# Optimization experiments

Measured on AMD Instinct MI355X. Metric: run time of the kernel, lower is better.

## Reference

```python
import jax, jax.numpy as jnp
import numpy as np

EPS = 1e-3  # keras LayerNormalization default epsilon

def _layernorm(x, g, b):
    mu = jnp.mean(x, axis=-1, keepdims=True)
    var = jnp.mean(jnp.square(x - mu), axis=-1, keepdims=True)
    return (x - mu) * jax.lax.rsqrt(var + EPS) * g + b

def setup_inputs() -> dict:
    key = jax.random.key(0)
    ks = jax.random.split(key, 12)
    B, T, C = 2, 2048, 768
    s = 0.02
    return {
        "x": jax.random.normal(ks[0], (B, T, C), jnp.float32),
        "ln1_g": jnp.ones((C,), jnp.float32), "ln1_b": jnp.zeros((C,), jnp.float32),
        "Wq": jax.random.normal(ks[1], (C, C), jnp.float32) * s, "bq": jnp.zeros((C,), jnp.float32),
        "Wk": jax.random.normal(ks[2], (C, C), jnp.float32) * s, "bk": jnp.zeros((C,), jnp.float32),
        "Wv": jax.random.normal(ks[3], (C, C), jnp.float32) * s, "bv": jnp.zeros((C,), jnp.float32),
        "ln2_g": jnp.ones((C,), jnp.float32), "ln2_b": jnp.zeros((C,), jnp.float32),
        "W1": jax.random.normal(ks[4], (C, 4 * C), jnp.float32) * s, "b1": jnp.zeros((4 * C,), jnp.float32),
        "W2": jax.random.normal(ks[5], (4 * C, C), jnp.float32) * s, "b2": jnp.zeros((C,), jnp.float32),
    }

def reference(x, ln1_g, ln1_b, Wq, bq, Wk, bk, Wv, bv, ln2_g, ln2_b, W1, b1, W2, b2):
    H = 12
    B, T, C = x.shape
    dh = C // H
    # pre-LN (note: original overwrites x with LN output before residual)
    x = _layernorm(x, ln1_g, ln1_b)
    q = (x @ Wq + bq).reshape(B, T, H, dh).transpose(0, 2, 1, 3)
    k = (x @ Wk + bk).reshape(B, T, H, dh).transpose(0, 2, 1, 3)
    v = (x @ Wv + bv).reshape(B, T, H, dh).transpose(0, 2, 1, 3)
    # original computes K @ Q^T (transpose_b on query)
    scores = jnp.einsum('bhid,bhjd->bhij', k, q) / jnp.sqrt(jnp.float32(dh))
    mask = jnp.tril(jnp.ones((T, T), bool))
    scores = jnp.where(mask, scores, -jnp.inf)
    p = jax.nn.softmax(scores, axis=-1)
    y = jnp.einsum('bhij,bhjd->bhid', p, v)  # [B,H,T,dh]
    y = y.transpose(0, 2, 1, 3).reshape(B, T, C)
    x = x + y
    h = _layernorm(x, ln2_g, ln2_b)
    h = jax.nn.gelu(h @ W1 + b1, approximate=False)
    h = h @ W2 + b2
    return x + h
```

## Files before the change

### kernel.cpp

```cpp
#include <hip/hip_runtime.h>
#include <hip/hip_bf16.h>
#include <cmath>


#define BB 2
#define TT 2048
#define CC 768
#define HH 12
#define DH 64
#define NROWS (BB*TT)

typedef __attribute__((ext_vector_type(8))) short bf16x8;
typedef __attribute__((ext_vector_type(4))) float f32x4;
typedef __attribute__((ext_vector_type(4))) unsigned short u16x4;

__device__ __forceinline__ unsigned short f2bf(float f){
  union { __hip_bfloat16 h; unsigned short u; } c;
  c.h = __float2bfloat16(f);
  return c.u;
}
__device__ __forceinline__ float bf2f(unsigned short u){
  union { unsigned int i; float f; } x; x.i = ((unsigned int)u) << 16; return x.f;
}
__device__ __forceinline__ int swz(int r, int c){
  int b = (r << 7) + (c << 1);
  b ^= (r & 7) << 4;
  return b >> 1;
}
__device__ __forceinline__ float wred_sum(float v){
  #pragma unroll
  for(int m = 1; m < 64; m <<= 1) v += __shfl_xor(v, m, 64);
  return v;
}
__device__ __forceinline__ float gelu_exact(float x){
  return 0.5f * x * (1.0f + erff(x * 0.70710678118654752f));
}
__device__ __forceinline__ void gload_lds16(const void* g, void* l){
  __builtin_amdgcn_global_load_lds((const __attribute__((address_space(1))) void*)g,
                                   (__attribute__((address_space(3))) void*)l, 16, 0, 0);
}
template<int N> __device__ __forceinline__ void waitcnt_vm(){
  if constexpr (N == 0)      asm volatile("s_waitcnt vmcnt(0)" ::: "memory");
  else if constexpr (N == 4) asm volatile("s_waitcnt vmcnt(4)" ::: "memory");
  else if constexpr (N == 8) asm volatile("s_waitcnt vmcnt(8)" ::: "memory");
  else static_assert(N == 0 || N == 4 || N == 8, "unsupported vmcnt");
}

__device__ __forceinline__ void tc_body(const float* __restrict__ in,
                                        unsigned short* __restrict__ out,
                                        int K, int N, int bx, int by,
                                        float (*tile)[33]){
  int n0 = bx * 32, k0 = by * 32;
  int t = threadIdx.x; int c = t & 31; int r0 = t >> 5;
  #pragma unroll
  for(int p = 0; p < 4; p++){
    int r = r0 + p * 8;
    tile[r][c] = in[(size_t)(k0 + r) * N + n0 + c];
  }
  __syncthreads();
  #pragma unroll
  for(int p = 0; p < 4; p++){
    int r = r0 + p * 8;
    out[(size_t)(n0 + r) * K + k0 + c] = f2bf(tile[c][r]);
  }
}

__device__ __forceinline__ void ln_body(const float* __restrict__ in,
                                        const float* __restrict__ gm,
                                        const float* __restrict__ bt,
                                        unsigned short* __restrict__ out_b,
                                        int r){
  int t = threadIdx.x;
  const float* row = in + (size_t)r * CC;
  float v0 = row[t], v1 = row[t + 256], v2 = row[t + 512];
  float s = wred_sum(v0 + v1 + v2);
  __shared__ float red[4];
  if((t & 63) == 0) red[t >> 6] = s;
  __syncthreads();
  float mu = (red[0] + red[1] + red[2] + red[3]) * (1.0f / CC);
  float d0 = v0 - mu, d1 = v1 - mu, d2 = v2 - mu;
  float q = wred_sum(d0 * d0 + d1 * d1 + d2 * d2);
  __shared__ float red2[4];
  if((t & 63) == 0) red2[t >> 6] = q;
  __syncthreads();
  float var = (red2[0] + red2[1] + red2[2] + red2[3]) * (1.0f / CC);
  float rinv = rsqrtf(var + 1e-3f);
  float o0 = d0 * rinv * gm[t]       + bt[t];
  float o1 = d1 * rinv * gm[t + 256] + bt[t + 256];
  float o2 = d2 * rinv * gm[t + 512] + bt[t + 512];
  size_t base = (size_t)r * CC;
  out_b[base + t] = f2bf(o0); out_b[base + t + 256] = f2bf(o1); out_b[base + t + 512] = f2bf(o2);
}

__global__ __launch_bounds__(256) void prep_ln_kernel(const float* __restrict__ Wq,
                                                      const float* __restrict__ Wk,
                                                      const float* __restrict__ Wv,
                                                      const float* __restrict__ W1,
                                                      const float* __restrict__ W2,
                                                      const float* __restrict__ bq,
                                                      const float* __restrict__ bk,
                                                      const float* __restrict__ bv,
                                                      const float* __restrict__ x,
                                                      const float* __restrict__ ln1g,
                                                      const float* __restrict__ ln1b,
                                                      unsigned short* __restrict__ wqkv,
                                                      unsigned short* __restrict__ w1t,
                                                      unsigned short* __restrict__ w2t,
                                                      float* __restrict__ bqkv,
                                                      unsigned short* __restrict__ xlnb){
  __shared__ float tile[32][33];
  int o = blockIdx.x;
  if(o < 1728){
    int z = o / 576, r = o % 576;
    const float* in = (z == 0) ? Wq : (z == 1) ? Wk : Wv;
    tc_body(in, wqkv + (size_t)z * CC * CC, CC, CC, r % 24, r / 24, tile);
  } else if(o < 4032){
    int r = o - 1728;
    tc_body(W1, w1t, CC, 4 * CC, r % 96, r / 96, tile);
  } else if(o < 6336){
    int r = o - 4032;
    tc_body(W2, w2t, 4 * CC, CC, r % 24, r / 24, tile);
  } else if(o < 6345){
    int i = (o - 6336) * 256 + threadIdx.x;
    if(i < 3 * CC) bqkv[i] = (i < CC) ? bq[i] : (i < 2 * CC) ? bk[i - CC] : bv[i - 2 * CC];
  } else {
    ln_body(x, ln1g, ln1b, xlnb, o - 6345);
  }
}

__global__ __launch_bounds__(256) void ln_kernel(const float* __restrict__ in,
                                                 const float* __restrict__ gm,
                                                 const float* __restrict__ bt,
                                                 unsigned short* __restrict__ out_b){
  ln_body(in, gm, bt, out_b, blockIdx.x);
}

template<int MODE, int TILE>
__global__ __launch_bounds__(256) void gemm_bt(const unsigned short* __restrict__ A,
                                               const unsigned short* __restrict__ Bt,
                                               const float* __restrict__ bias,
                                               const float* __restrict__ resid,
                                               void* __restrict__ outp,
                                               int M, int N, int K){
  constexpr int F = TILE / 32;
  constexpr int R = TILE / 32;
  constexpr int NLD = 2 * R;
  __shared__ unsigned short As[2][TILE * 64];
  __shared__ unsigned short Bs[2][TILE * 64];
  int m0 = blockIdx.y * TILE, n0 = blockIdx.x * TILE;
  int t = threadIdx.x; int w = t >> 6; int l = t & 63;
  int g = l >> 4; int lc = l & 15;
  int wm = w >> 1, wn = w & 1;
  f32x4 zero4 = {0.f, 0.f, 0.f, 0.f};
  f32x4 acc[F][F];
  #pragma unroll
  for(int mi = 0; mi < F; mi++)
    #pragma unroll
    for(int ni = 0; ni < F; ni++) acc[mi][ni] = zero4;

  auto stage = [&](int ks, int cb){
    #pragma unroll
    for(int p = 0; p < R; p++){
      int e = (w * R + p) * 512 + l * 8;
      int r = e >> 6, clin = e & 63;
      int csrc = clin ^ ((r & 7) << 3);
      gload_lds16(A  + (size_t)(m0 + r) * K + ks + csrc, &As[cb][(w * R + p) * 512]);
      gload_lds16(Bt + (size_t)(n0 + r) * K + ks + csrc, &Bs[cb][(w * R + p) * 512]);
    }
  };

  int nt = K >> 6;
  stage(0, 0);
  if(nt > 1) stage(64, 1);
  for(int ti = 0; ti < nt; ti++){
    if(ti + 1 < nt) waitcnt_vm<NLD>(); else waitcnt_vm<0>();
    __builtin_amdgcn_s_barrier();
    int cur = ti & 1;
    #pragma unroll
    for(int kk = 0; kk < 2; kk++){
      bf16x8 af[F], bfv[F];
      #pragma unroll
      for(int mi = 0; mi < F; mi++) af[mi]  = *(const bf16x8*)&As[cur][swz(wm * (TILE / 2) + mi * 16 + lc, kk * 32 + g * 8)];
      #pragma unroll
      for(int ni = 0; ni < F; ni++) bfv[ni] = *(const bf16x8*)&Bs[cur][swz(wn * (TILE / 2) + ni * 16 + lc, kk * 32 + g * 8)];
      #pragma unroll
      for(int mi = 0; mi < F; mi++)
        #pragma unroll
        for(int ni = 0; ni < F; ni++)
          acc[mi][ni] = __builtin_amdgcn_mfma_f32_16x16x32_bf16(af[mi], bfv[ni], acc[mi][ni], 0, 0, 0);
    }
    __builtin_amdgcn_s_barrier();
    if(ti + 2 < nt) stage((ti + 2) << 6, cur);
  }
  #pragma unroll
  for(int mi = 0; mi < F; mi++)
    #pragma unroll
    for(int ni = 0; ni < F; ni++){
      int col = n0 + wn * (TILE / 2) + ni * 16 + lc;
      float bvv = bias[col];
      #pragma unroll
      for(int rr = 0; rr < 4; rr++){
        int row = m0 + wm * (TILE / 2) + mi * 16 + g * 4 + rr;
        float v = acc[mi][ni][rr] + bvv;
        size_t idx = (size_t)row * N + col;
        if(MODE == 1) v = gelu_exact(v);
        if(MODE == 2) ((float*)outp)[idx] = v + resid[idx];
        else          ((unsigned short*)outp)[idx] = f2bf(v);
      }
    }
}

__global__ __launch_bounds__(256) void transpose_v(const unsigned short* __restrict__ qkv,
                                                   unsigned short* __restrict__ vt){
  __shared__ unsigned short tile[64][65];
  int t0 = blockIdx.x * 64; int bh = blockIdx.y;
  int b = bh / HH, h = bh % HH;
  int t = threadIdx.x;
  #pragma unroll
  for(int p = 0; p < 2; p++){
    int idx = p * 256 + t; int r = idx >> 3; int c = (idx & 7) * 8;
    bf16x8 v = *(const bf16x8*)(qkv + (size_t)(b * TT + t0 + r) * (3 * CC) + 2 * CC + h * DH + c);
    #pragma unroll
    for(int e = 0; e < 8; e++) tile[r][c + e] = (unsigned short)v[e];
  }
  __syncthreads();
  #pragma unroll
  for(int p = 0; p < 2; p++){
    int idx = p * 256 + t; int d = idx >> 3; int c = (idx & 7) * 8;
    bf16x8 v;
    #pragma unroll
    for(int e = 0; e < 8; e++) v[e] = (short)tile[c + e][d];
    *(bf16x8*)(vt + (size_t)(bh * DH + d) * TT + t0 + c) = v;
  }
}

__global__ __launch_bounds__(256) void attn_kernel(const unsigned short* __restrict__ qkv,
                                                   const unsigned short* __restrict__ vt,
                                                   const unsigned short* __restrict__ xlnb,
                                                   float* __restrict__ x1){
  __shared__ unsigned short Aq[2][64 * 64];
  __shared__ unsigned short Vs[2][64 * 64];
  __shared__ unsigned short Ps[4][16 * 64];
  int o = blockIdx.x;
  int xcd = o & 7, qq = o >> 3;
  int head = xcd * 3 + (qq % 3);
  int bx = 31 - qq / 3;
  int b = head / HH, h = head % HH;
  int t = threadIdx.x; int w = t >> 6; int l = t & 63;
  int g = l >> 4, lc = l & 15;
  int i0w = bx * 64 + w * 16;
  int irow = i0w + lc;
  unsigned short* pw = &Ps[w][0];
  const float SC = 0.125f * 1.44269504f;

  int rl = l >> 3;
  int csrc = ((l & 7) * 8) ^ (rl * 8);

  bf16x8 bk[2];
  #pragma unroll
  for(int kk = 0; kk < 2; kk++)
    bk[kk] = *(const bf16x8*)(qkv + (size_t)(b * TT + irow) * (3 * CC) + CC + h * DH + kk * 32 + g * 8);

  float m_ = 0.0f, lsum = 0.f;
  f32x4 zero4 = {0.f, 0.f, 0.f, 0.f};
  f32x4 o4[4];
  #pragma unroll
  for(int ds = 0; ds < 4; ds++) o4[ds] = zero4;

  int NJT_w = (i0w + 16 + 63) >> 6;
  int NJTmax = bx + 1;

  auto stage = [&](int j0, int cb){
    #pragma unroll
    for(int p = 0; p < 2; p++){
      int sgi = w * 2 + p;
      int row = sgi * 8 + rl;
      gload_lds16(qkv + (size_t)(b * TT + j0 + row) * (3 * CC) + h * DH + csrc, &Aq[cb][sgi * 512]);
      gload_lds16(vt  + (size_t)(head * DH + row) * TT + j0 + csrc,             &Vs[cb][sgi * 512]);
    }
  };

  stage(0, 0);
  if(NJTmax > 1) stage(64, 1);

  for(int jt = 0; jt < NJTmax; jt++){
    int j0 = jt * 64;
    int buf = jt & 1;
    if(jt + 1 < NJTmax) waitcnt_vm<4>(); else waitcnt_vm<0>();
    __builtin_amdgcn_s_barrier();
    if(jt < NJT_w){
      f32x4 s[4];
      __builtin_amdgcn_s_setprio(1);
      #pragma unroll
      for(int js = 0; js < 4; js++){
        s[js] = zero4;
        #pragma unroll
        for(int kk = 0; kk < 2; kk++){
          bf16x8 aq = *(const bf16x8*)&Aq[buf][swz(js * 16 + lc, kk * 32 + g * 8)];
          s[js] = __builtin_amdgcn_mfma_f32_16x16x32_bf16(aq, bk[kk], s[js], 0, 0, 0);
        }
      }
      __builtin_amdgcn_s_setprio(0);
      if(j0 + 63 > i0w){
        #pragma unroll
        for(int js = 0; js < 4; js++)
          #pragma unroll
          for(int rr = 0; rr < 4; rr++){
            int j = j0 + js * 16 + g * 4 + rr;
            if(j > irow) s[js][rr] = -1e30f;
          }
      }
      float nmSC = -m_ * SC;
      f32x4 p[4];
      float rsum = 0.f;
      #pragma unroll
      for(int js = 0; js < 4; js++)
        #pragma unroll
        for(int rr = 0; rr < 4; rr++){
          float pv = exp2f(fmaf(s[js][rr], SC, nmSC));
          p[js][rr] = pv;
          rsum += pv;
        }
      rsum += __shfl_xor(rsum, 16, 64);
      rsum += __shfl_xor(rsum, 32, 64);
      if(__builtin_expect(__any(!(rsum < 1e30f)), 0)){
        float mx = -1e30f;
        #pragma unroll
        for(int js = 0; js < 4; js++)
          #pragma unroll
          for(int rr = 0; rr < 4; rr++) mx = fmaxf(mx, s[js][rr]);
        mx = fmaxf(mx, __shfl_xor(mx, 16, 64));
        mx = fmaxf(mx, __shfl_xor(mx, 32, 64));
        float mn = fmaxf(m_, mx);
        float al = exp2f((m_ - mn) * SC);
        m_ = mn;
        lsum *= al;
        #pragma unroll
        for(int rr = 0; rr < 4; rr++){
          float alb = __shfl(al, g * 4 + rr, 64);
          #pragma unroll
          for(int ds = 0; ds < 4; ds++) o4[ds][rr] *= alb;
        }
        nmSC = -m_ * SC;
        rsum = 0.f;
        #pragma unroll
        for(int js = 0; js < 4; js++)
          #pragma unroll
          for(int rr = 0; rr < 4; rr++){
            float pv = exp2f(fmaf(s[js][rr], SC, nmSC));
            p[js][rr] = pv;
            rsum += pv;
          }
        rsum += __shfl_xor(rsum, 16, 64);
        rsum += __shfl_xor(rsum, 32, 64);
      }
      lsum += rsum;
      #pragma unroll
      for(int js = 0; js < 4; js++){
        u16x4 pk;
        #pragma unroll
        for(int rr = 0; rr < 4; rr++) pk[rr] = f2bf(p[js][rr]);
        *(u16x4*)&pw[swz(lc, js * 16 + g * 4)] = pk;
      }
      bf16x8 pa[2];
      #pragma unroll
      for(int kk = 0; kk < 2; kk++)
        pa[kk] = *(const bf16x8*)&pw[swz(lc, kk * 32 + g * 8)];
      __builtin_amdgcn_s_setprio(1);
      #pragma unroll
      for(int ds = 0; ds < 4; ds++)
        #pragma unroll
        for(int kk = 0; kk < 2; kk++){
          bf16x8 vb = *(const bf16x8*)&Vs[buf][swz(ds * 16 + lc, kk * 32 + g * 8)];
          o4[ds] = __builtin_amdgcn_mfma_f32_16x16x32_bf16(pa[kk], vb, o4[ds], 0, 0, 0);
        }
      __builtin_amdgcn_s_setprio(0);
    }
    __builtin_amdgcn_s_barrier();
    if(jt + 2 < NJTmax) stage((jt + 2) * 64, buf);
  }
  #pragma unroll
  for(int rr = 0; rr < 4; rr++){
    float lsb = __shfl(lsum, g * 4 + rr, 64);
    float rinv = 1.0f / lsb;
    int ig = i0w + g * 4 + rr;
    #pragma unroll
    for(int ds = 0; ds < 4; ds++){
      int col = h * DH + ds * 16 + lc;
      size_t idx = (size_t)(b * TT + ig) * CC + col;
      x1[idx] = bf2f(xlnb[idx]) + o4[ds][rr] * rinv;
    }
  }
}

extern "C" void kernel_launch(void* const* d_in, const int* in_sizes, int n_in,
                              void* d_out, int out_size, void* d_ws, size_t ws_size,
                              hipStream_t stream){
  const float* x    = (const float*)d_in[0];
  const float* ln1g = (const float*)d_in[1];
  const float* ln1b = (const float*)d_in[2];
  const float* Wq   = (const float*)d_in[3];
  const float* bq   = (const float*)d_in[4];
  const float* Wk   = (const float*)d_in[5];
  const float* bk   = (const float*)d_in[6];
  const float* Wv   = (const float*)d_in[7];
  const float* bv   = (const float*)d_in[8];
  const float* ln2g = (const float*)d_in[9];
  const float* ln2b = (const float*)d_in[10];
  const float* W1   = (const float*)d_in[11];
  const float* b1   = (const float*)d_in[12];
  const float* W2   = (const float*)d_in[13];
  const float* b2   = (const float*)d_in[14];

  char* ws = (char*)d_ws;
  unsigned short* xlnb = (unsigned short*)(ws + 12582912);
  float*          x1   = (float*)(ws + 18874368);
  unsigned short* hln2 = (unsigned short*)(ws + 31457280);
  unsigned short* wqkv = (unsigned short*)(ws + 37748736);
  float*          bqkv = (float*)(ws + 41287680);
  unsigned short* w1t  = (unsigned short*)(ws + 41296896);
  unsigned short* w2t  = (unsigned short*)(ws + 46015488);
  unsigned short* qkv  = (unsigned short*)(ws + 50734080);
  unsigned short* vt   = (unsigned short*)(ws + 69608448);
  unsigned short* mlp1 = (unsigned short*)(ws + 50734080);

  prep_ln_kernel<<<dim3(6345 + NROWS), 256, 0, stream>>>(Wq, Wk, Wv, W1, W2, bq, bk, bv,
                                                         x, ln1g, ln1b,
                                                         wqkv, w1t, w2t, bqkv, xlnb);

  gemm_bt<0, 128><<<dim3(18, 32), 256, 0, stream>>>(xlnb, wqkv, bqkv, nullptr, qkv, NROWS, 3 * CC, CC);

  transpose_v<<<dim3(TT / 64, BB * HH), 256, 0, stream>>>(qkv, vt);

  attn_kernel<<<dim3(768), 256, 0, stream>>>(qkv, vt, xlnb, x1);

  ln_kernel<<<NROWS, 256, 0, stream>>>(x1, ln2g, ln2b, hln2);

  gemm_bt<1, 128><<<dim3(24, 32), 256, 0, stream>>>(hln2, w1t, b1, nullptr, mlp1, NROWS, 4 * CC, CC);

  gemm_bt<2, 64><<<dim3(12, 64), 256, 0, stream>>>(mlp1, w2t, b2, x1, d_out, NROWS, CC, 4 * CC);

  (void)in_sizes; (void)n_in; (void)out_size; (void)ws_size;
}
```

Measured before the change: 173.2 us.

## Split attention KV range across two blocks, fuse V transpose and LN2 combine

Attention now launches twice as many blocks, each handling half of the causal key range for a query tile and writing partial outputs plus row max and sum. A new combine kernel merges the two partials with log-sum-exp weights, adds the residual and applies LayerNorm 2, replacing the separate ln_kernel. The QKV GEMM gains a mode that writes V directly in transposed layout, removing the transpose_v kernel. This targets load imbalance from causal masking and cuts two launches, at the cost of extra partial-result traffic through global memory and bf16 rounding of the unnormalized partial outputs.

```diff
diff --git a/kernel.cpp b/kernel.cpp
--- a/kernel.cpp
+++ b/kernel.cpp
@@ -9,6 +9,7 @@
 #define HH 12
 #define DH 64
 #define NROWS (BB*TT)
+#define NHEADS (BB*HH)
 
 typedef __attribute__((ext_vector_type(8))) short bf16x8;
 typedef __attribute__((ext_vector_type(4))) float f32x4;
@@ -45,6 +46,8 @@
   else if constexpr (N == 8) asm volatile("s_waitcnt vmcnt(8)" ::: "memory");
   else static_assert(N == 0 || N == 4 || N == 8, "unsupported vmcnt");
 }
+
+#define SCLOG2 (0.125f * 1.44269504f)
 
 __device__ __forceinline__ void tc_body(const float* __restrict__ in,
                                         unsigned short* __restrict__ out,
@@ -128,19 +131,13 @@
   }
 }
 
-__global__ __launch_bounds__(256) void ln_kernel(const float* __restrict__ in,
-                                                 const float* __restrict__ gm,
-                                                 const float* __restrict__ bt,
-                                                 unsigned short* __restrict__ out_b){
-  ln_body(in, gm, bt, out_b, blockIdx.x);
-}
-
 template<int MODE, int TILE>
 __global__ __launch_bounds__(256) void gemm_bt(const unsigned short* __restrict__ A,
                                                const unsigned short* __restrict__ Bt,
                                                const float* __restrict__ bias,
                                                const float* __restrict__ resid,
                                                void* __restrict__ outp,
+                                               unsigned short* __restrict__ vt,
                                                int M, int N, int K){
   constexpr int F = TILE / 32;
   constexpr int R = TILE / 32;
@@ -198,60 +195,52 @@
     for(int ni = 0; ni < F; ni++){
       int col = n0 + wn * (TILE / 2) + ni * 16 + lc;
       float bvv = bias[col];
-      #pragma unroll
-      for(int rr = 0; rr < 4; rr++){
-        int row = m0 + wm * (TILE / 2) + mi * 16 + g * 4 + rr;
-        float v = acc[mi][ni][rr] + bvv;
-        size_t idx = (size_t)row * N + col;
-        if(MODE == 1) v = gelu_exact(v);
-        if(MODE == 2) ((float*)outp)[idx] = v + resid[idx];
-        else          ((unsigned short*)outp)[idx] = f2bf(v);
+      if(MODE == 3 && col >= 2 * CC){
+        int hh = (col - 2 * CC) >> 6, d = (col - 2 * CC) & 63;
+        int rowb = m0 + wm * (TILE / 2) + mi * 16 + g * 4;
+        int bb = rowb >> 11, tb = rowb & 2047;
+        u16x4 pk;
+        #pragma unroll
+        for(int rr = 0; rr < 4; rr++) pk[rr] = f2bf(acc[mi][ni][rr] + bvv);
+        *(u16x4*)&vt[(((size_t)bb * HH + hh) * DH + d) * TT + tb] = pk;
+      } else {
+        #pragma unroll
+        for(int rr = 0; rr < 4; rr++){
+          int row = m0 + wm * (TILE / 2) + mi * 16 + g * 4 + rr;
+          float v = acc[mi][ni][rr] + bvv;
+          size_t idx = (size_t)row * N + col;
+          if(MODE == 1) v = gelu_exact(v);
+          if(MODE == 2) ((float*)outp)[idx] = v + resid[idx];
+          else          ((unsigned short*)outp)[idx] = f2bf(v);
+        }
       }
     }
 }
 
-__global__ __launch_bounds__(256) void transpose_v(const unsigned short* __restrict__ qkv,
-                                                   unsigned short* __restrict__ vt){
-  __shared__ unsigned short tile[64][65];
-  int t0 = blockIdx.x * 64; int bh = blockIdx.y;
-  int b = bh / HH, h = bh % HH;
-  int t = threadIdx.x;
-  #pragma unroll
-  for(int p = 0; p < 2; p++){
-    int idx = p * 256 + t; int r = idx >> 3; int c = (idx & 7) * 8;
-    bf16x8 v = *(const bf16x8*)(qkv + (size_t)(b * TT + t0 + r) * (3 * CC) + 2 * CC + h * DH + c);
-    #pragma unroll
-    for(int e = 0; e < 8; e++) tile[r][c + e] = (unsigned short)v[e];
-  }
-  __syncthreads();
-  #pragma unroll
-  for(int p = 0; p < 2; p++){
-    int idx = p * 256 + t; int d = idx >> 3; int c = (idx & 7) * 8;
-    bf16x8 v;
-    #pragma unroll
-    for(int e = 0; e < 8; e++) v[e] = (short)tile[c + e][d];
-    *(bf16x8*)(vt + (size_t)(bh * DH + d) * TT + t0 + c) = v;
-  }
-}
-
 __global__ __launch_bounds__(256) void attn_kernel(const unsigned short* __restrict__ qkv,
                                                    const unsigned short* __restrict__ vt,
-                                                   const unsigned short* __restrict__ xlnb,
-                                                   float* __restrict__ x1){
+                                                   unsigned short* __restrict__ po,
+                                                   float* __restrict__ pl,
+                                                   float* __restrict__ pm){
   __shared__ unsigned short Aq[2][64 * 64];
   __shared__ unsigned short Vs[2][64 * 64];
   __shared__ unsigned short Ps[4][16 * 64];
   int o = blockIdx.x;
   int xcd = o & 7, qq = o >> 3;
   int head = xcd * 3 + (qq % 3);
-  int bx = 31 - qq / 3;
+  int r_ = qq / 3;
+  int bx = 31 - (r_ >> 1);
+  int sp = r_ & 1;
   int b = head / HH, h = head % HH;
   int t = threadIdx.x; int w = t >> 6; int l = t & 63;
   int g = l >> 4, lc = l & 15;
   int i0w = bx * 64 + w * 16;
   int irow = i0w + lc;
   unsigned short* pw = &Ps[w][0];
-  const float SC = 0.125f * 1.44269504f;
+
+  int hh = (bx + 2) >> 1;
+  int js0 = sp ? hh : 0;
+  int js1 = sp ? (bx + 1) : hh;
 
   int rl = l >> 3;
   int csrc = ((l & 7) * 8) ^ (rl * 8);
@@ -266,9 +255,6 @@
   f32x4 o4[4];
   #pragma unroll
   for(int ds = 0; ds < 4; ds++) o4[ds] = zero4;
-
-  int NJT_w = (i0w + 16 + 63) >> 6;
-  int NJTmax = bx + 1;
 
   auto stage = [&](int j0, int cb){
     #pragma unroll
@@ -280,15 +266,15 @@
     }
   };
 
-  stage(0, 0);
-  if(NJTmax > 1) stage(64, 1);
-
-  for(int jt = 0; jt < NJTmax; jt++){
-    int j0 = jt * 64;
-    int buf = jt & 1;
-    if(jt + 1 < NJTmax) waitcnt_vm<4>(); else waitcnt_vm<0>();
-    __builtin_amdgcn_s_barrier();
-    if(jt < NJT_w){
+  if(js0 < js1){
+    stage(js0 * 64, js0 & 1);
+    if(js0 + 1 < js1) stage((js0 + 1) * 64, (js0 + 1) & 1);
+
+    for(int jt = js0; jt < js1; jt++){
+      int j0 = jt * 64;
+      int buf = jt & 1;
+      if(jt + 1 < js1) waitcnt_vm<4>(); else waitcnt_vm<0>();
+      __builtin_amdgcn_s_barrier();
       f32x4 s[4];
       __builtin_amdgcn_s_setprio(1);
       #pragma unroll
@@ -310,14 +296,14 @@
             if(j > irow) s[js][rr] = -1e30f;
           }
       }
-      float nmSC = -m_ * SC;
+      float nmSC = -m_ * SCLOG2;
       f32x4 p[4];
       float rsum = 0.f;
       #pragma unroll
       for(int js = 0; js < 4; js++)
         #pragma unroll
         for(int rr = 0; rr < 4; rr++){
-          float pv = exp2f(fmaf(s[js][rr], SC, nmSC));
+          float pv = exp2f(fmaf(s[js][rr], SCLOG2, nmSC));
           p[js][rr] = pv;
           rsum += pv;
         }
@@ -332,7 +318,7 @@
         mx = fmaxf(mx, __shfl_xor(mx, 16, 64));
         mx = fmaxf(mx, __shfl_xor(mx, 32, 64));
         float mn = fmaxf(m_, mx);
-        float al = exp2f((m_ - mn) * SC);
+        float al = exp2f((m_ - mn) * SCLOG2);
         m_ = mn;
         lsum *= al;
         #pragma unroll
@@ -341,13 +327,13 @@
           #pragma unroll
           for(int ds = 0; ds < 4; ds++) o4[ds][rr] *= alb;
         }
-        nmSC = -m_ * SC;
+        nmSC = -m_ * SCLOG2;
         rsum = 0.f;
         #pragma unroll
         for(int js = 0; js < 4; js++)
           #pragma unroll
           for(int rr = 0; rr < 4; rr++){
-            float pv = exp2f(fmaf(s[js][rr], SC, nmSC));
+            float pv = exp2f(fmaf(s[js][rr], SCLOG2, nmSC));
             p[js][rr] = pv;
             rsum += pv;
           }
@@ -375,22 +361,67 @@
           o4[ds] = __builtin_amdgcn_mfma_f32_16x16x32_bf16(pa[kk], vb, o4[ds], 0, 0, 0);
         }
       __builtin_amdgcn_s_setprio(0);
+      __builtin_amdgcn_s_barrier();
+      if(jt + 2 < js1) stage((jt + 2) * 64, buf);
     }
-    __builtin_amdgcn_s_barrier();
-    if(jt + 2 < NJTmax) stage((jt + 2) * 64, buf);
-  }
+  }
+  size_t pobase = (size_t)sp * (NHEADS * TT * DH) + (size_t)head * TT * DH;
   #pragma unroll
   for(int rr = 0; rr < 4; rr++){
-    float lsb = __shfl(lsum, g * 4 + rr, 64);
-    float rinv = 1.0f / lsb;
     int ig = i0w + g * 4 + rr;
     #pragma unroll
-    for(int ds = 0; ds < 4; ds++){
-      int col = h * DH + ds * 16 + lc;
-      size_t idx = (size_t)(b * TT + ig) * CC + col;
-      x1[idx] = bf2f(xlnb[idx]) + o4[ds][rr] * rinv;
-    }
-  }
+    for(int ds = 0; ds < 4; ds++)
+      po[pobase + (size_t)ig * DH + ds * 16 + lc] = f2bf(o4[ds][rr]);
+  }
+  if(g == 0){
+    size_t pidx = (size_t)sp * (NHEADS * TT) + (size_t)head * TT + i0w + lc;
+    pl[pidx] = lsum;
+    pm[pidx] = m_;
+  }
+}
+
+__global__ __launch_bounds__(256) void combine_ln2(const unsigned short* __restrict__ po,
+                                                   const float* __restrict__ pl,
+                                                   const float* __restrict__ pm,
+                                                   const unsigned short* __restrict__ xlnb,
+                                                   const float* __restrict__ gm,
+                                                   const float* __restrict__ bt,
+                                                   float* __restrict__ x1,
+                                                   unsigned short* __restrict__ hln2){
+  int r = blockIdx.x; int t = threadIdx.x;
+  int b = r >> 11, i = r & 2047;
+  float v[3];
+  #pragma unroll
+  for(int p = 0; p < 3; p++){
+    int c = t + p * 256;
+    int h = c >> 6, d = c & 63;
+    size_t pidx = ((size_t)(b * HH + h)) * TT + i;
+    float m0v = pm[pidx], m1v = pm[pidx + NHEADS * TT];
+    float l0 = pl[pidx],  l1 = pl[pidx + NHEADS * TT];
+    float M = fmaxf(m0v, m1v);
+    float w0 = exp2f((m0v - M) * SCLOG2), w1 = exp2f((m1v - M) * SCLOG2);
+    float p0 = bf2f(po[pidx * DH + d]);
+    float p1 = bf2f(po[(size_t)NHEADS * TT * DH + pidx * DH + d]);
+    float att = (p0 * w0 + p1 * w1) / (l0 * w0 + l1 * w1);
+    v[p] = bf2f(xlnb[(size_t)r * CC + c]) + att;
+  }
+  float s = wred_sum(v[0] + v[1] + v[2]);
+  __shared__ float red[4];
+  if((t & 63) == 0) red[t >> 6] = s;
+  __syncthreads();
+  float mu = (red[0] + red[1] + red[2] + red[3]) * (1.0f / CC);
+  float d0 = v[0] - mu, d1 = v[1] - mu, d2 = v[2] - mu;
+  float q = wred_sum(d0 * d0 + d1 * d1 + d2 * d2);
+  __shared__ float red2[4];
+  if((t & 63) == 0) red2[t >> 6] = q;
+  __syncthreads();
+  float var = (red2[0] + red2[1] + red2[2] + red2[3]) * (1.0f / CC);
+  float rinv = rsqrtf(var + 1e-3f);
+  size_t base = (size_t)r * CC;
+  x1[base + t] = v[0]; x1[base + t + 256] = v[1]; x1[base + t + 512] = v[2];
+  hln2[base + t]       = f2bf(d0 * rinv * gm[t]       + bt[t]);
+  hln2[base + t + 256] = f2bf(d1 * rinv * gm[t + 256] + bt[t + 256]);
+  hln2[base + t + 512] = f2bf(d2 * rinv * gm[t + 512] + bt[t + 512]);
 }
 
 extern "C" void kernel_launch(void* const* d_in, const int* in_sizes, int n_in,
@@ -413,6 +444,7 @@
   const float* b2   = (const float*)d_in[14];
 
   char* ws = (char*)d_ws;
+  unsigned short* po   = (unsigned short*)(ws + 0);
   unsigned short* xlnb = (unsigned short*)(ws + 12582912);
   float*          x1   = (float*)(ws + 18874368);
   unsigned short* hln2 = (unsigned short*)(ws + 31457280);
@@ -422,23 +454,23 @@
   unsigned short* w2t  = (unsigned short*)(ws + 46015488);
   unsigned short* qkv  = (unsigned short*)(ws + 50734080);
   unsigned short* vt   = (unsigned short*)(ws + 69608448);
+  float*          pl   = (float*)(ws + 75899904);
+  float*          pm   = (float*)(ws + 76293120);
   unsigned short* mlp1 = (unsigned short*)(ws + 50734080);
 
   prep_ln_kernel<<<dim3(6345 + NROWS), 256, 0, stream>>>(Wq, Wk, Wv, W1, W2, bq, bk, bv,
                                                          x, ln1g, ln1b,
                                                          wqkv, w1t, w2t, bqkv, xlnb);
 
-  gemm_bt<0, 128><<<dim3(18, 32), 256, 0, stream>>>(xlnb, wqkv, bqkv, nullptr, qkv, NROWS, 3 * CC, CC);
-
-  transpose_v<<<dim3(TT / 64, BB * HH), 256, 0, stream>>>(qkv, vt);
-
-  attn_kernel<<<dim3(768), 256, 0, stream>>>(qkv, vt, xlnb, x1);
-
-  ln_kernel<<<NROWS, 256, 0, stream>>>(x1, ln2g, ln2b, hln2);
-
-  gemm_bt<1, 128><<<dim3(24, 32), 256, 0, stream>>>(hln2, w1t, b1, nullptr, mlp1, NROWS, 4 * CC, CC);
-
-  gemm_bt<2, 64><<<dim3(12, 64), 256, 0, stream>>>(mlp1, w2t, b2, x1, d_out, NROWS, CC, 4 * CC);
+  gemm_bt<3, 128><<<dim3(18, 32), 256, 0, stream>>>(xlnb, wqkv, bqkv, nullptr, qkv, vt, NROWS, 3 * CC, CC);
+
+  attn_kernel<<<dim3(1536), 256, 0, stream>>>(qkv, vt, po, pl, pm);
+
+  combine_ln2<<<dim3(NROWS), 256, 0, stream>>>(po, pl, pm, xlnb, ln2g, ln2b, x1, hln2);
+
+  gemm_bt<1, 128><<<dim3(24, 32), 256, 0, stream>>>(hln2, w1t, b1, nullptr, mlp1, nullptr, NROWS, 4 * CC, CC);
+
+  gemm_bt<2, 64><<<dim3(12, 64), 256, 0, stream>>>(mlp1, w2t, b2, x1, d_out, nullptr, NROWS, CC, 4 * CC);
 
   (void)in_sizes; (void)n_in; (void)out_size; (void)ws_size;
 }
```

After: 163.3 us. -5.7%, faster.
